# Kernel optimization log

Hardware: AMD Instinct MI355X
Metric: run time of the kernel (lower is better)

## Reference

```python
import jax, jax.numpy as jnp
import numpy as np


def setup_inputs() -> dict:
    key = jax.random.key(0)
    ks = jax.random.split(key, 8)
    B, M, C, H, W = 2, 16, 256, 64, 64
    T = 1024  # transformer_dim
    return {
        "transformer_output": jax.random.normal(ks[0], (B, T), dtype=jnp.float32),
        "residual_maps": jax.random.normal(ks[1], (B, M, C, H, W), dtype=jnp.float32),
        "Wq": jax.random.normal(ks[2], (C, T), dtype=jnp.float32) * 0.02,
        "bq": jnp.zeros((C,), dtype=jnp.float32),
        "Wk": jax.random.normal(ks[3], (C, C), dtype=jnp.float32) * 0.02,
        "bk": jnp.zeros((C,), dtype=jnp.float32),
        "Wv": jax.random.normal(ks[4], (C, C), dtype=jnp.float32) * 0.02,
        "bv": jnp.zeros((C,), dtype=jnp.float32),
    }


def reference(transformer_output, residual_maps, Wq, bq, Wk, bk, Wv, bv):
    # residual_maps: [B, M, C, H, W]; single query per batch element.
    B, M, C, H, W = residual_maps.shape
    scale = C ** (-0.5)
    # Linear query projection: [B, C]
    q = transformer_output @ Wq.T + bq
    # 1x1 conv == per-pixel channel matmul: [B, M, C, H, W]
    keys = jnp.einsum("oc,bmchw->bmohw", Wk, residual_maps) + bk[None, None, :, None, None]
    values = jnp.einsum("oc,bmchw->bmohw", Wv, residual_maps) + bv[None, None, :, None, None]
    # Single-query dot-product scores per (map, pixel): [B, M, H, W]
    scores = jnp.einsum("bc,bmchw->bmhw", q, keys) * scale
    # Temporal softmax over num_maps at each spatial position
    probs = jax.nn.softmax(scores, axis=1)
    # Softmax-weighted sum of value maps: [B, C, H, W]
    out = jnp.einsum("bmhw,bmchw->bchw", probs, values)
    return out
```

## Files before the change

### kernel.cpp

```cpp
#include <hip/hip_runtime.h>

#define SCALE 0.0625f

typedef __attribute__((ext_vector_type(4))) float f32x4;
typedef __attribute__((ext_vector_type(8))) short s16x8;

__device__ __forceinline__ unsigned short f2bf(float x) {
    unsigned u = __float_as_uint(x);
    u = u + 0x7FFF + ((u >> 16) & 1);
    return (unsigned short)(u >> 16);
}

__global__ __launch_bounds__(256) void prep1_kernel(
    const float* __restrict__ TO,
    const float* __restrict__ Wq,
    const float* __restrict__ bq,
    const float* __restrict__ Wv,
    float* __restrict__ qbuf,
    unsigned short* __restrict__ WvB)
{
    const int blk = blockIdx.x;
    const int t   = threadIdx.x;
    if (blk < 16) {
        const int b    = blk >> 3;
        const int rblk = blk & 7;
        const int wv = t >> 6, l = t & 63;
        const float4* Wq4 = (const float4*)Wq;
        const float4* TO4 = (const float4*)TO;
        for (int rr = 0; rr < 8; ++rr) {
            const int c = rblk * 32 + wv * 8 + rr;
            float acc = 0.f;
#pragma unroll
            for (int i = 0; i < 4; ++i) {
                float4 wq = Wq4[c * 256 + i * 64 + l];
                float4 tv = TO4[b * 256 + i * 64 + l];
                acc = fmaf(wq.x, tv.x, acc);
                acc = fmaf(wq.y, tv.y, acc);
                acc = fmaf(wq.z, tv.z, acc);
                acc = fmaf(wq.w, tv.w, acc);
            }
#pragma unroll
            for (int mask = 1; mask < 64; mask <<= 1)
                acc += __shfl_xor(acc, mask, 64);
            if (l == 0) qbuf[b * 256 + c] = acc + bq[c];
        }
    } else {
        const int idx = blk - 16;
#pragma unroll
        for (int i = 0; i < 4; ++i) {
            const int e = idx * 4096 + i * 1024 + t * 4;
            const float4 f = ((const float4*)Wv)[e >> 2];
            ushort4 o;
            o.x = f2bf(f.x); o.y = f2bf(f.y);
            o.z = f2bf(f.z); o.w = f2bf(f.w);
            *(ushort4*)(WvB + e) = o;
        }
    }
}

__global__ __launch_bounds__(256) void prep2_kernel(
    const float* __restrict__ qbuf,
    const float* __restrict__ Wk,
    float* __restrict__ qks)
{
    const int blk = blockIdx.x;
    const int t   = threadIdx.x;
    const int b = blk >> 3, j = blk & 7;
    const int col = t & 31, chunk = t >> 5;
    const int cp = j * 32 + col;
    float partial = 0.f;
#pragma unroll 8
    for (int cc = 0; cc < 32; ++cc) {
        const int c = chunk * 32 + cc;
        partial = fmaf(qbuf[b * 256 + c], Wk[c * 256 + cp], partial);
    }
    __shared__ float r2[8][32];
    r2[chunk][col] = partial;
    __syncthreads();
    if (t < 32) {
        float s = 0.f;
#pragma unroll
        for (int k = 0; k < 8; ++k) s += r2[k][t];
        qks[b * 256 + j * 32 + t] = SCALE * s;
    }
}

__global__ __launch_bounds__(512, 1) void fused_kernel(
    const float* __restrict__ X,
    const float* __restrict__ qks,
    const unsigned short* __restrict__ WvB,
    const float* __restrict__ bv,
    float* __restrict__ out)
{
    const int t   = threadIdx.x;
    const int blk = blockIdx.x;
    const int b   = blk >> 7;
    const int hw0 = (blk & 127) << 5;

    __shared__ float pl[16][32];
    __shared__ float invl[32];
    __shared__ float slab[256 * 36];

    {
        const int px = t & 31, ms = t >> 5;
        const float* __restrict__ Xr = X + ((b * 16 + ms) * 256) * 4096 + hw0 + px;
        const float* __restrict__ qr = qks + b * 256;
        float a0 = 0.f, a1 = 0.f, a2 = 0.f, a3 = 0.f;
        float a4 = 0.f, a5 = 0.f, a6 = 0.f, a7 = 0.f;
#pragma unroll 4
        for (int c = 0; c < 256; c += 8) {
            a0 = fmaf(qr[c + 0], Xr[(c + 0) * 4096], a0);
            a1 = fmaf(qr[c + 1], Xr[(c + 1) * 4096], a1);
            a2 = fmaf(qr[c + 2], Xr[(c + 2) * 4096], a2);
            a3 = fmaf(qr[c + 3], Xr[(c + 3) * 4096], a3);
            a4 = fmaf(qr[c + 4], Xr[(c + 4) * 4096], a4);
            a5 = fmaf(qr[c + 5], Xr[(c + 5) * 4096], a5);
            a6 = fmaf(qr[c + 6], Xr[(c + 6) * 4096], a6);
            a7 = fmaf(qr[c + 7], Xr[(c + 7) * 4096], a7);
        }
        const float s = ((a0 + a1) + (a2 + a3)) + ((a4 + a5) + (a6 + a7));
        pl[ms][px] = __expf(s);
        __syncthreads();
        if (t < 32) {
            float sm = 0.f;
#pragma unroll
            for (int m = 0; m < 16; ++m) sm += pl[m][t];
            invl[t] = 1.0f / sm;
        }
        __syncthreads();
        pl[ms][px] *= invl[px];
        __syncthreads();
    }

    const int p4 = t & 7;
    const int cg = t >> 3;
    const float4* X4 = (const float4*)X;
    const int base0 = (b * 16) * 262144 + (hw0 >> 2) + p4;

    float4 v[3][4];
    float4 wx[4];
#pragma unroll
    for (int k = 0; k < 4; ++k) wx[k] = make_float4(0.f, 0.f, 0.f, 0.f);

#pragma unroll
    for (int k = 0; k < 4; ++k)
        v[0][k] = X4[base0 + (cg + 64 * k) * 1024];
#pragma unroll
    for (int k = 0; k < 4; ++k)
        v[1][k] = X4[base0 + 262144 + (cg + 64 * k) * 1024];

#pragma unroll
    for (int m = 0; m < 16; ++m) {
        const int cur = m % 3;
        const int nxt = (m + 2) % 3;
        if (m < 14) {
#pragma unroll
            for (int k = 0; k < 4; ++k)
                v[nxt][k] = X4[base0 + (m + 2) * 262144 + (cg + 64 * k) * 1024];
        }
        const float4 pm = *(const float4*)&pl[m][4 * p4];
#pragma unroll
        for (int k = 0; k < 4; ++k) {
            wx[k].x = fmaf(pm.x, v[cur][k].x, wx[k].x);
            wx[k].y = fmaf(pm.y, v[cur][k].y, wx[k].y);
            wx[k].z = fmaf(pm.z, v[cur][k].z, wx[k].z);
            wx[k].w = fmaf(pm.w, v[cur][k].w, wx[k].w);
        }
    }

#pragma unroll
    for (int k = 0; k < 4; ++k)
        *(float4*)&slab[(cg + 64 * k) * 36 + 4 * p4] = wx[k];
    __syncthreads();

    const int w    = t >> 6;
    const int ph   = w & 1;
    const int cot  = w >> 1;
    const int lane = t & 63;
    const int pxl  = lane & 15;
    const int quad = lane >> 4;
    const int px   = 16 * ph + pxl;

    f32x4 acc[4];
#pragma unroll
    for (int i = 0; i < 4; ++i) {
        const int tt = 4 * cot + i;
#pragma unroll
        for (int r = 0; r < 4; ++r)
            acc[i][r] = bv[16 * tt + quad * 4 + r];
    }

#pragma unroll
    for (int ks = 0; ks < 8; ++ks) {
        s16x8 bfr;
#pragma unroll
        for (int j = 0; j < 8; ++j)
            bfr[j] = (short)f2bf(slab[(ks * 32 + quad * 8 + j) * 36 + px]);
#pragma unroll
        for (int i = 0; i < 4; ++i) {
            const int tt = 4 * cot + i;
            const s16x8 afr =
                *(const s16x8*)(WvB + (16 * tt + pxl) * 256 + ks * 32 + quad * 8);
            acc[i] = __builtin_amdgcn_mfma_f32_16x16x32_bf16(afr, bfr, acc[i],
                                                             0, 0, 0);
        }
    }

    const int obase = b * 1048576 + hw0;
#pragma unroll
    for (int i = 0; i < 4; ++i) {
        const int tt = 4 * cot + i;
#pragma unroll
        for (int r = 0; r < 4; ++r) {
            const int co = 16 * tt + quad * 4 + r;
            out[obase + co * 4096 + px] = acc[i][r];
        }
    }
}

extern "C" void kernel_launch(void* const* d_in, const int* in_sizes, int n_in,
                              void* d_out, int out_size, void* d_ws, size_t ws_size,
                              hipStream_t stream) {
    const float* TO = (const float*)d_in[0];
    const float* X  = (const float*)d_in[1];
    const float* Wq = (const float*)d_in[2];
    const float* bq = (const float*)d_in[3];
    const float* Wk = (const float*)d_in[4];
    const float* Wv = (const float*)d_in[6];
    const float* bv = (const float*)d_in[7];
    float* out = (float*)d_out;
    float* ws  = (float*)d_ws;

    float*          qbuf = ws;
    float*          qks  = ws + 512;
    unsigned short* WvB  = (unsigned short*)(ws + 1024);

    hipLaunchKernelGGL(prep1_kernel, dim3(32), dim3(256), 0, stream,
                       TO, Wq, bq, Wv, qbuf, WvB);
    hipLaunchKernelGGL(prep2_kernel, dim3(16), dim3(256), 0, stream,
                       qbuf, Wk, qks);
    hipLaunchKernelGGL(fused_kernel, dim3(256), dim3(512), 0, stream,
                       X, qks, WvB, bv, out);
}
```

Before: 249.2 us.

## Split fused attention kernel into scores, softmax, weighted-sum and conv stages

The single fused kernel, which ran only 256 blocks and streamed X twice inside each block, is split into four kernels. The new kernels compute partial scores over channel chunks (512 blocks), reduce them with a softmax, form the probability-weighted sum of X with coalesced float4 loads, and then apply the Wv projection with MFMA. The aim is better parallelism and memory coalescing on the two X passes. The cost is extra launches and round trips through global workspace for partial scores, probabilities and the weighted sum.

```diff
diff --git a/kernel.cpp b/kernel.cpp
--- a/kernel.cpp
+++ b/kernel.cpp
@@ -85,9 +85,150 @@
     }
 }
 
-__global__ __launch_bounds__(512, 1) void fused_kernel(
+__global__ __launch_bounds__(256) void scores_part_kernel(
     const float* __restrict__ X,
     const float* __restrict__ qks,
+    float* __restrict__ part)
+{
+    const int blk = blockIdx.x;
+    const int bm  = blk >> 4;
+    const int cc  = (blk >> 1) & 7;
+    const int ph  = blk & 1;
+    const int b   = bm >> 4;
+    const int t   = threadIdx.x;
+
+    const float4* __restrict__ X4 =
+        (const float4*)X + bm * 262144 + cc * 32768 + ph * 512 + t;
+    const float* __restrict__ qr = qks + b * 256 + cc * 32;
+
+    float4 a[2][2];
+#pragma unroll
+    for (int s = 0; s < 2; ++s)
+#pragma unroll
+        for (int r = 0; r < 2; ++r) a[s][r] = make_float4(0, 0, 0, 0);
+
+#pragma unroll
+    for (int c = 0; c < 32; c += 2) {
+        const float4 x00 = X4[(c + 0) * 1024];
+        const float4 x01 = X4[(c + 0) * 1024 + 256];
+        const float4 x10 = X4[(c + 1) * 1024];
+        const float4 x11 = X4[(c + 1) * 1024 + 256];
+        const float q0 = qr[c + 0], q1 = qr[c + 1];
+        a[0][0].x = fmaf(q0, x00.x, a[0][0].x);
+        a[0][0].y = fmaf(q0, x00.y, a[0][0].y);
+        a[0][0].z = fmaf(q0, x00.z, a[0][0].z);
+        a[0][0].w = fmaf(q0, x00.w, a[0][0].w);
+        a[1][0].x = fmaf(q0, x01.x, a[1][0].x);
+        a[1][0].y = fmaf(q0, x01.y, a[1][0].y);
+        a[1][0].z = fmaf(q0, x01.z, a[1][0].z);
+        a[1][0].w = fmaf(q0, x01.w, a[1][0].w);
+        a[0][1].x = fmaf(q1, x10.x, a[0][1].x);
+        a[0][1].y = fmaf(q1, x10.y, a[0][1].y);
+        a[0][1].z = fmaf(q1, x10.z, a[0][1].z);
+        a[0][1].w = fmaf(q1, x10.w, a[0][1].w);
+        a[1][1].x = fmaf(q1, x11.x, a[1][1].x);
+        a[1][1].y = fmaf(q1, x11.y, a[1][1].y);
+        a[1][1].z = fmaf(q1, x11.z, a[1][1].z);
+        a[1][1].w = fmaf(q1, x11.w, a[1][1].w);
+    }
+
+    float4* __restrict__ P4 = (float4*)part + (cc * 32 + bm) * 1024 + ph * 512 + t;
+    float4 s0, s1;
+    s0.x = a[0][0].x + a[0][1].x;  s0.y = a[0][0].y + a[0][1].y;
+    s0.z = a[0][0].z + a[0][1].z;  s0.w = a[0][0].w + a[0][1].w;
+    s1.x = a[1][0].x + a[1][1].x;  s1.y = a[1][0].y + a[1][1].y;
+    s1.z = a[1][0].z + a[1][1].z;  s1.w = a[1][0].w + a[1][1].w;
+    P4[0]   = s0;
+    P4[256] = s1;
+}
+
+__global__ __launch_bounds__(256) void softmax_kernel(
+    const float* __restrict__ part,
+    float* __restrict__ probs)
+{
+    const int blk = blockIdx.x;
+    const int b   = blk >> 4;
+    const int px  = ((blk & 15) << 8) + threadIdx.x;
+    float e[16];
+    float tot = 0.f;
+#pragma unroll
+    for (int m = 0; m < 16; ++m) {
+        float s = 0.f;
+#pragma unroll
+        for (int cc = 0; cc < 8; ++cc)
+            s += part[(cc * 32 + b * 16 + m) * 4096 + px];
+        e[m] = __expf(s);
+        tot += e[m];
+    }
+    const float inv = 1.0f / tot;
+#pragma unroll
+    for (int m = 0; m < 16; ++m)
+        probs[(b * 16 + m) * 4096 + px] = e[m] * inv;
+}
+
+__global__ __launch_bounds__(256) void wx_kernel(
+    const float* __restrict__ X,
+    const float* __restrict__ probs,
+    float* __restrict__ wxg)
+{
+    const int blk = blockIdx.x;
+    const int b   = blk >> 7;
+    const int cp  = blk & 127;
+    const int t   = threadIdx.x;
+
+    const float4* __restrict__ X4 = (const float4*)X;
+    const float4* __restrict__ P4 = (const float4*)probs;
+
+    const int xbase = b * 16 * 262144 + 2 * cp * 1024 + t;
+    const int pbase = b * 16 * 1024 + t;
+
+    float4 wxa[2][4];
+#pragma unroll
+    for (int ci = 0; ci < 2; ++ci)
+#pragma unroll
+        for (int sg = 0; sg < 4; ++sg) wxa[ci][sg] = make_float4(0,0,0,0);
+
+    float4 v[2][2][4];
+    float4 pv[2][4];
+#pragma unroll
+    for (int sg = 0; sg < 4; ++sg) {
+        v[0][0][sg] = X4[xbase + 0 * 1024 + sg * 256];
+        v[0][1][sg] = X4[xbase + 1 * 1024 + sg * 256];
+        pv[0][sg]   = P4[pbase + sg * 256];
+    }
+
+#pragma unroll
+    for (int m = 0; m < 16; ++m) {
+        const int buf = m & 1, nxt = buf ^ 1;
+        if (m < 15) {
+#pragma unroll
+            for (int sg = 0; sg < 4; ++sg) {
+                v[nxt][0][sg] = X4[xbase + (m + 1) * 262144 + 0 * 1024 + sg * 256];
+                v[nxt][1][sg] = X4[xbase + (m + 1) * 262144 + 1 * 1024 + sg * 256];
+                pv[nxt][sg]   = P4[pbase + (m + 1) * 1024 + sg * 256];
+            }
+        }
+#pragma unroll
+        for (int ci = 0; ci < 2; ++ci)
+#pragma unroll
+            for (int sg = 0; sg < 4; ++sg) {
+                wxa[ci][sg].x = fmaf(pv[buf][sg].x, v[buf][ci][sg].x, wxa[ci][sg].x);
+                wxa[ci][sg].y = fmaf(pv[buf][sg].y, v[buf][ci][sg].y, wxa[ci][sg].y);
+                wxa[ci][sg].z = fmaf(pv[buf][sg].z, v[buf][ci][sg].z, wxa[ci][sg].z);
+                wxa[ci][sg].w = fmaf(pv[buf][sg].w, v[buf][ci][sg].w, wxa[ci][sg].w);
+            }
+    }
+
+    float4* __restrict__ W4 = (float4*)wxg;
+#pragma unroll
+    for (int ci = 0; ci < 2; ++ci)
+#pragma unroll
+        for (int sg = 0; sg < 4; ++sg)
+            W4[(b * 256 + 2 * cp + ci) * 1024 + sg * 256 + t] = wxa[ci][sg];
+}
+
+__global__ __launch_bounds__(512, 1) void conv_kernel(
+    const float* __restrict__ wxg,
     const unsigned short* __restrict__ WvB,
     const float* __restrict__ bv,
     float* __restrict__ out)
@@ -97,80 +238,17 @@
     const int b   = blk >> 7;
     const int hw0 = (blk & 127) << 5;
 
-    __shared__ float pl[16][32];
-    __shared__ float invl[32];
     __shared__ float slab[256 * 36];
 
-    {
-        const int px = t & 31, ms = t >> 5;
-        const float* __restrict__ Xr = X + ((b * 16 + ms) * 256) * 4096 + hw0 + px;
-        const float* __restrict__ qr = qks + b * 256;
-        float a0 = 0.f, a1 = 0.f, a2 = 0.f, a3 = 0.f;
-        float a4 = 0.f, a5 = 0.f, a6 = 0.f, a7 = 0.f;
-#pragma unroll 4
-        for (int c = 0; c < 256; c += 8) {
-            a0 = fmaf(qr[c + 0], Xr[(c + 0) * 4096], a0);
-            a1 = fmaf(qr[c + 1], Xr[(c + 1) * 4096], a1);
-            a2 = fmaf(qr[c + 2], Xr[(c + 2) * 4096], a2);
-            a3 = fmaf(qr[c + 3], Xr[(c + 3) * 4096], a3);
-            a4 = fmaf(qr[c + 4], Xr[(c + 4) * 4096], a4);
-            a5 = fmaf(qr[c + 5], Xr[(c + 5) * 4096], a5);
-            a6 = fmaf(qr[c + 6], Xr[(c + 6) * 4096], a6);
-            a7 = fmaf(qr[c + 7], Xr[(c + 7) * 4096], a7);
-        }
-        const float s = ((a0 + a1) + (a2 + a3)) + ((a4 + a5) + (a6 + a7));
-        pl[ms][px] = __expf(s);
-        __syncthreads();
-        if (t < 32) {
-            float sm = 0.f;
-#pragma unroll
-            for (int m = 0; m < 16; ++m) sm += pl[m][t];
-            invl[t] = 1.0f / sm;
-        }
-        __syncthreads();
-        pl[ms][px] *= invl[px];
-        __syncthreads();
-    }
-
-    const int p4 = t & 7;
-    const int cg = t >> 3;
-    const float4* X4 = (const float4*)X;
-    const int base0 = (b * 16) * 262144 + (hw0 >> 2) + p4;
-
-    float4 v[3][4];
-    float4 wx[4];
-#pragma unroll
-    for (int k = 0; k < 4; ++k) wx[k] = make_float4(0.f, 0.f, 0.f, 0.f);
-
-#pragma unroll
-    for (int k = 0; k < 4; ++k)
-        v[0][k] = X4[base0 + (cg + 64 * k) * 1024];
-#pragma unroll
-    for (int k = 0; k < 4; ++k)
-        v[1][k] = X4[base0 + 262144 + (cg + 64 * k) * 1024];
-
-#pragma unroll
-    for (int m = 0; m < 16; ++m) {
-        const int cur = m % 3;
-        const int nxt = (m + 2) % 3;
-        if (m < 14) {
-#pragma unroll
-            for (int k = 0; k < 4; ++k)
-                v[nxt][k] = X4[base0 + (m + 2) * 262144 + (cg + 64 * k) * 1024];
-        }
-        const float4 pm = *(const float4*)&pl[m][4 * p4];
-#pragma unroll
-        for (int k = 0; k < 4; ++k) {
-            wx[k].x = fmaf(pm.x, v[cur][k].x, wx[k].x);
-            wx[k].y = fmaf(pm.y, v[cur][k].y, wx[k].y);
-            wx[k].z = fmaf(pm.z, v[cur][k].z, wx[k].z);
-            wx[k].w = fmaf(pm.w, v[cur][k].w, wx[k].w);
-        }
-    }
-
-#pragma unroll
-    for (int k = 0; k < 4; ++k)
-        *(float4*)&slab[(cg + 64 * k) * 36 + 4 * p4] = wx[k];
+#pragma unroll
+    for (int i = 0; i < 4; ++i) {
+        const int idx = t + 512 * i;
+        const int c   = idx >> 3;
+        const int px4 = idx & 7;
+        const float4 v =
+            ((const float4*)wxg)[(b * 256 + c) * 1024 + (hw0 >> 2) + px4];
+        *(float4*)&slab[c * 36 + 4 * px4] = v;
+    }
     __syncthreads();
 
     const int w    = t >> 6;
@@ -231,14 +309,23 @@
     float* out = (float*)d_out;
     float* ws  = (float*)d_ws;
 
-    float*          qbuf = ws;
-    float*          qks  = ws + 512;
-    unsigned short* WvB  = (unsigned short*)(ws + 1024);
+    float*          qbuf  = ws;
+    float*          qks   = ws + 512;
+    unsigned short* WvB   = (unsigned short*)(ws + 1024);
+    float*          part  = ws + 33792;
+    float*          probs = ws + 33792 + 1048576;
+    float*          wxg   = ws + 33792 + 1048576 + 131072;
 
     hipLaunchKernelGGL(prep1_kernel, dim3(32), dim3(256), 0, stream,
                        TO, Wq, bq, Wv, qbuf, WvB);
     hipLaunchKernelGGL(prep2_kernel, dim3(16), dim3(256), 0, stream,
                        qbuf, Wk, qks);
-    hipLaunchKernelGGL(fused_kernel, dim3(256), dim3(512), 0, stream,
-                       X, qks, WvB, bv, out);
-}
+    hipLaunchKernelGGL(scores_part_kernel, dim3(512), dim3(256), 0, stream,
+                       X, qks, part);
+    hipLaunchKernelGGL(softmax_kernel, dim3(32), dim3(256), 0, stream,
+                       part, probs);
+    hipLaunchKernelGGL(wx_kernel, dim3(256), dim3(256), 0, stream,
+                       X, probs, wxg);
+    hipLaunchKernelGGL(conv_kernel, dim3(256), dim3(512), 0, stream,
+                       wxg, WvB, bv, out);
+}
```

New measurement: 283.8 us. 1.14x slower.
